# Performance work log

Hardware: AMD Instinct MI355X
Metric: run time of the kernel (lower is better)

## Reference

```python
import jax, jax.numpy as jnp
import numpy as np
import itertools
from jax import lax

B, CIN, COUT, RES, NH = 32, 512, 512, 56, 8
STRIDE = RES // 7  # 8 -> post-stride grid is 7x7 (N=49)
HD = COUT // NH    # 64


def _affine(x, s, b):  # BatchNorm2d in inference form (per-channel scale/shift)
    return x * s[None, :, None, None] + b[None, :, None, None]


def _conv1x1(x, w):  # w: [O, C]
    return jnp.einsum('oc,bchw->bohw', w, x)


def _conv3x3(x, w, stride, groups):
    return lax.conv_general_dilated(
        x, w, window_strides=(stride, stride), padding=[(1, 1), (1, 1)],
        feature_group_count=groups, dimension_numbers=('NCHW', 'OIHW', 'NCHW'))


def _bias_idx():
    points = list(itertools.product(range(7), range(7)))
    offsets, idxs = {}, []
    for p1 in points:
        for p2 in points:
            off = (abs(p1[0] - p2[0]), abs(p1[1] - p2[1]))
            if off not in offsets:
                offsets[off] = len(offsets)
            idxs.append(offsets[off])
    return np.array(idxs, dtype=np.int32).reshape(49, 49), len(offsets)


def setup_inputs() -> dict:
    key = jax.random.key(0)
    ks = jax.random.split(key, 24)
    idx_np, n_off = _bias_idx()  # n_off = 49
    rn = lambda k, sh, sc: jax.random.normal(k, sh, dtype=jnp.float32) * sc
    return {
        'x': rn(ks[0], (B, CIN, RES, RES), 1.0),
        'dw_w': rn(ks[1], (CIN, 1, 3, 3), 0.2),
        'bn0_s': 1.0 + rn(ks[2], (CIN,), 0.05), 'bn0_b': rn(ks[3], (CIN,), 0.05),
        'wq': rn(ks[4], (COUT, CIN), 0.03),
        'bnq_s': 1.0 + rn(ks[5], (COUT,), 0.05), 'bnq_b': rn(ks[6], (COUT,), 0.05),
        'wk': rn(ks[7], (COUT, CIN), 0.03),
        'bnk_s': 1.0 + rn(ks[8], (COUT,), 0.05), 'bnk_b': rn(ks[9], (COUT,), 0.05),
        'wv': rn(ks[10], (COUT, CIN), 0.03),
        'bnv_s': 1.0 + rn(ks[11], (COUT,), 0.05), 'bnv_b': rn(ks[12], (COUT,), 0.05),
        'loc_w': rn(ks[13], (COUT, COUT // NH, 3, 3), 0.05), 'loc_b': rn(ks[14], (COUT,), 0.02),
        'bnl_s': 1.0 + rn(ks[15], (COUT,), 0.05), 'bnl_b': rn(ks[16], (COUT,), 0.05),
        'th1': rn(ks[17], (NH, NH), 0.3), 'th2': rn(ks[18], (NH, NH), 0.3),
        'logit_scale': jnp.log(10.0) * jnp.ones((NH, 1, 1), dtype=jnp.float32),
        'ab': rn(ks[19], (NH, n_off), 0.02),
        'wo': rn(ks[20], (COUT, COUT), 0.03),
        'bno_s': 1.0 + rn(ks[21], (COUT,), 0.05), 'bno_b': rn(ks[22], (COUT,), 0.05),
        'bias_idx': jnp.array(idx_np),
    }


def reference(x, dw_w, bn0_s, bn0_b, wq, bnq_s, bnq_b, wk, bnk_s, bnk_b,
              wv, bnv_s, bnv_b, loc_w, loc_b, bnl_s, bnl_b, th1, th2,
              logit_scale, ab, wo, bno_s, bno_b, bias_idx):
    # stride_conv: depthwise 3x3 stride-8 + BN -> [B, C, 7, 7]
    x = _affine(_conv3x3(x, dw_w, STRIDE, CIN), bn0_s, bn0_b)
    Bc, C, H, W = x.shape
    N = H * W  # 49
    q = _affine(_conv1x1(x, wq), bnq_s, bnq_b).reshape(Bc, NH, HD, N).transpose(0, 1, 3, 2)  # [B,H,N,d]
    k = _affine(_conv1x1(x, wk), bnk_s, bnk_b).reshape(Bc, NH, HD, N)                        # [B,H,d,N]
    v4 = _affine(_conv1x1(x, wv), bnv_s, bnv_b)                                              # [B,Cout,7,7]
    v_local = _affine(_conv3x3(v4, loc_w, 1, NH) + loc_b[None, :, None, None], bnl_s, bnl_b)
    v = v4.reshape(Bc, NH, HD, N).transpose(0, 1, 3, 2)                                      # [B,H,N,d]
    # faithful to source: q normalized over head_dim, k normalized over token axis (last)
    qn = q / jnp.maximum(jnp.linalg.norm(q, axis=-1, keepdims=True), 1e-12)
    kn = k / jnp.maximum(jnp.linalg.norm(k, axis=-1, keepdims=True), 1e-12)
    ls = jnp.exp(jnp.minimum(logit_scale, jnp.log(100.0)))  # clamp max then exp
    attn = jnp.einsum('bhnd,bhdm->bhnm', qn, kn) * ls + ab[:, bias_idx]  # [B,H,49,49]
    attn = jnp.einsum('ij,bjnm->binm', th1, attn)   # talking head 1
    attn = jax.nn.softmax(attn, axis=-1)
    attn = jnp.einsum('ij,bjnm->binm', th2, attn)   # talking head 2
    out = jnp.einsum('bhnm,bhmd->bhnd', attn, v)    # [B,H,N,d]
    out = out.transpose(0, 1, 3, 2).reshape(Bc, COUT, H, W) + v_local
    out = jax.image.resize(out, (Bc, COUT, H * STRIDE, W * STRIDE), method='bilinear')
    out = out * jax.nn.relu6(out + 3.0) / 6.0       # Hardswish
    return _affine(_conv1x1(out, wo), bno_s, bno_b)
```

## Files before the change

kernel.cpp:

```cpp
#include <hip/hip_runtime.h>
#include <hip/hip_bf16.h>
#include <stdint.h>

typedef short short8 __attribute__((ext_vector_type(8)));
typedef float f32x4 __attribute__((ext_vector_type(4)));

#define NB    32
#define NC    512
#define NHD   8
#define HDD   64
#define N7    49
#define RES   56
#define P56   3136
#define NTOK  1568
#define NTOKP 1664
#define NBIG  100352
#define KDIM  512
#define KLOC  576

__device__ __forceinline__ void gload_lds16(const __hip_bfloat16* g, __hip_bfloat16* l) {
  __builtin_amdgcn_global_load_lds(
      (const __attribute__((address_space(1))) void*)g,
      (__attribute__((address_space(3))) void*)l, 16, 0, 0);
}

__global__ __launch_bounds__(256) void k_stride_cvt(
    const float* __restrict__ x, const float* __restrict__ dw,
    const float* __restrict__ s0, const float* __restrict__ b0,
    __hip_bfloat16* __restrict__ xs,
    const float* __restrict__ c0, const float* __restrict__ c1,
    const float* __restrict__ c2, const float* __restrict__ c3,
    const float* __restrict__ c4,
    __hip_bfloat16* __restrict__ d0, __hip_bfloat16* __restrict__ d1,
    __hip_bfloat16* __restrict__ d2, __hip_bfloat16* __restrict__ d3,
    __hip_bfloat16* __restrict__ d4) {
  const int bid = blockIdx.x, t = threadIdx.x;
  if (bid >= 4096) {
    const long base = (long)(bid - 4096) * 2048;
#pragma unroll
    for (int j = 0; j < 8; ++j) {
      long i = base + t + j * 256;
      const float* s; __hip_bfloat16* d; long off;
      if (i >= 1048576)      { s = c4; d = d4; off = i - 1048576; }
      else if (i >= 786432)  { s = c3; d = d3; off = i - 786432; }
      else if (i >= 524288)  { s = c2; d = d2; off = i - 524288; }
      else if (i >= 262144)  { s = c1; d = d1; off = i - 262144; }
      else                   { s = c0; d = d0; off = i; }
      d[off] = __float2bfloat16(s[off]);
    }
    return;
  }
  const int b = bid >> 7, cig = bid & 127;
  const int sub = t >> 6, lane = t & 63;
  const int ci = cig * 4 + sub;
  __shared__ float rows[4][21][56];
  const float* xp = x + ((size_t)(b * NC + ci)) * RES * RES;
  for (int r = lane; r < 21 * 56; r += 64) {
    int rr = r / 56, cc = r - rr * 56;
    int oh = rr / 3, kh = rr - oh * 3;
    int ih = oh * 8 + kh - 1;
    rows[sub][rr][cc] = (ih >= 0) ? xp[ih * 56 + cc] : 0.f;
  }
  float w[9];
#pragma unroll
  for (int j = 0; j < 9; ++j) w[j] = dw[ci * 9 + j];
  const float sc = s0[ci], bi = b0[ci];
  __syncthreads();
  if (lane < 49) {
    const int oh = lane / 7, ow = lane - oh * 7;
    float acc = 0.f;
#pragma unroll
    for (int kh = 0; kh < 3; ++kh)
#pragma unroll
      for (int kw = 0; kw < 3; ++kw) {
        int col = ow * 8 + kw - 1;
        float v = (col >= 0) ? rows[sub][oh * 3 + kh][col] : 0.f;
        acc += v * w[kh * 3 + kw];
      }
    xs[(size_t)(b * 49 + lane) * NC + ci] = __float2bfloat16(acc * sc + bi);
  }
}

__global__ __launch_bounds__(512) void k_gemm_big(
    const __hip_bfloat16* __restrict__ A,
    const __hip_bfloat16* __restrict__ Bm,
    const float* __restrict__ scale, const float* __restrict__ bias,
    float* __restrict__ out) {
  __shared__ __align__(16) __hip_bfloat16 lsA[2][256 * 32];
  __shared__ __align__(16) __hip_bfloat16 lsB[2][256 * 32];
  const int t = threadIdx.x;
  const int cpx = gridDim.x >> 3;
  const int nid = (blockIdx.x & 7) * cpx + (blockIdx.x >> 3);
  const int m0 = (nid & 1) * 256, n0 = (nid >> 1) * 256;

  const int lane = t & 63, wid = t >> 6;
  const int wm = (wid >> 2) * 128, wn = (wid & 3) * 64;
  const int fr = lane & 15, fq = lane >> 4;
  const int rslot = (fq ^ ((fr >> 1) & 3)) * 8;

  const int srow = t >> 2;
  const int scol = ((t & 3) ^ ((t >> 3) & 3)) * 8;
  const __hip_bfloat16* Ab = A  + (size_t)(m0 + srow) * KDIM + scol;
  const __hip_bfloat16* Bb = Bm + (size_t)(n0 + srow) * KDIM + scol;

  const f32x4 fz = {0.f, 0.f, 0.f, 0.f};
  f32x4 acc[8][4];
#pragma unroll
  for (int i = 0; i < 8; ++i)
#pragma unroll
    for (int j = 0; j < 4; ++j) acc[i][j] = fz;

#define STA(tile, call) gload_lds16(Ab + (tile) * 32 + (size_t)(call) * 128 * KDIM, \
                                    lsA[(tile) & 1] + (call) * 4096 + wid * 512)
#define STB(tile, call) gload_lds16(Bb + (tile) * 32 + (size_t)(call) * 128 * KDIM, \
                                    lsB[(tile) & 1] + (call) * 4096 + wid * 512)

  STA(0, 0); STA(0, 1); STB(0, 0); STB(0, 1);
  STA(1, 0); STA(1, 1); STB(1, 0); STB(1, 1);

#pragma unroll 1
  for (int tt = 0; tt < 16; ++tt) {
    if (tt < 15) asm volatile("s_waitcnt vmcnt(4)" ::: "memory");
    else         asm volatile("s_waitcnt vmcnt(0)" ::: "memory");
    __builtin_amdgcn_sched_barrier(0);
    __builtin_amdgcn_s_barrier();
    __builtin_amdgcn_sched_barrier(0);

    const __hip_bfloat16* lA = lsA[tt & 1];
    const __hip_bfloat16* lB = lsB[tt & 1];
    short8 af[4], ag[4], bf[4];
#pragma unroll
    for (int i = 0; i < 4; ++i)
      af[i] = *(const short8*)(lA + (wm + i * 16 + fr) * 32 + rslot);
#pragma unroll
    for (int i = 0; i < 4; ++i)
      ag[i] = *(const short8*)(lA + (wm + 64 + i * 16 + fr) * 32 + rslot);
#pragma unroll
    for (int j = 0; j < 4; ++j)
      bf[j] = *(const short8*)(lB + (wn + j * 16 + fr) * 32 + rslot);
    __builtin_amdgcn_s_setprio(1);
#pragma unroll
    for (int i = 0; i < 4; ++i)
#pragma unroll
      for (int j = 0; j < 4; ++j)
        acc[i][j] = __builtin_amdgcn_mfma_f32_16x16x32_bf16(af[i], bf[j], acc[i][j], 0, 0, 0);
#pragma unroll
    for (int i = 0; i < 4; ++i)
#pragma unroll
      for (int j = 0; j < 4; ++j)
        acc[4 + i][j] = __builtin_amdgcn_mfma_f32_16x16x32_bf16(ag[i], bf[j], acc[4 + i][j], 0, 0, 0);
    __builtin_amdgcn_s_setprio(0);

    __builtin_amdgcn_sched_barrier(0);
    __builtin_amdgcn_s_barrier();
    __builtin_amdgcn_sched_barrier(0);
    if (tt < 14) { STA(tt + 2, 0); STA(tt + 2, 1); STB(tt + 2, 0); STB(tt + 2, 1); }
  }
#undef STA
#undef STB

#pragma unroll
  for (int mi = 0; mi < 8; ++mi) {
#pragma unroll
    for (int ni = 0; ni < 4; ++ni) {
      const int gn = n0 + wn + ni * 16 + fr;
      const int outer = gn / P56;
      const int ii = gn - outer * P56;
#pragma unroll
      for (int r = 0; r < 4; ++r) {
        const int co = m0 + wm + mi * 16 + fq * 4 + r;
        out[((size_t)outer * NC + co) * P56 + ii] = acc[mi][ni][r] * scale[co] + bias[co];
      }
    }
  }
}

__global__ __launch_bounds__(256) void k_gemm_qkv(
    const __hip_bfloat16* __restrict__ wqb, const __hip_bfloat16* __restrict__ wkb,
    const __hip_bfloat16* __restrict__ wvb, const __hip_bfloat16* __restrict__ xs,
    const float* __restrict__ sq, const float* __restrict__ bq,
    const float* __restrict__ sk, const float* __restrict__ bk,
    const float* __restrict__ sv, const float* __restrict__ bv,
    float* __restrict__ qb, float* __restrict__ kb, float* __restrict__ vb) {
  __shared__ __align__(16) __hip_bfloat16 lsA[2][128 * 32];
  __shared__ __align__(16) __hip_bfloat16 lsB[2][128 * 32];
  const int t = threadIdx.x;
  const int nwg = gridDim.x;
  const int orig = blockIdx.x;
  const int q = nwg >> 3, r = nwg & 7;
  const int xcd = orig & 7, pos = orig >> 3;
  const int nid = (xcd < r ? xcd * (q + 1) : r * (q + 1) + (xcd - r) * q) + pos;
  const int mt = nid % 12, nt = nid / 12;
  const int n0 = nt * 128, m0 = (mt & 3) * 128, sel = mt >> 2;

  const __hip_bfloat16* A = (sel == 0 ? wqb : sel == 1 ? wkb : wvb);
  const float* scale = (sel == 0 ? sq : sel == 1 ? sk : sv);
  const float* bias  = (sel == 0 ? bq : sel == 1 ? bk : bv);
  float* out = (sel == 0 ? qb : sel == 1 ? kb : vb);

  const int lane = t & 63, wid = t >> 6;
  const int wm = (wid >> 1) * 64, wn = (wid & 1) * 64;
  const int fr = lane & 15, fq = lane >> 4;
  const int rslot = (fq ^ ((fr >> 1) & 3)) * 8;
  const int srow = t >> 2;
  const int scol = ((t & 3) ^ ((t >> 3) & 3)) * 8;
  const __hip_bfloat16* Ab = A  + (size_t)(m0 + srow) * KDIM + scol;
  const __hip_bfloat16* Bb = xs + (size_t)(n0 + srow) * KDIM + scol;

  const f32x4 fz = {0.f, 0.f, 0.f, 0.f};
  f32x4 acc[4][4];
#pragma unroll
  for (int i = 0; i < 4; ++i)
#pragma unroll
    for (int j = 0; j < 4; ++j) acc[i][j] = fz;

#define STG_QKV(tile)                                                   \
  do {                                                                  \
    const int kof = (tile) * 32; const int bb = (tile) & 1;             \
    gload_lds16(Ab + kof,                       lsA[bb] + wid * 512);   \
    gload_lds16(Ab + kof + (size_t)64 * KDIM,   lsA[bb] + 2048 + wid * 512); \
    gload_lds16(Bb + kof,                       lsB[bb] + wid * 512);   \
    gload_lds16(Bb + kof + (size_t)64 * KDIM,   lsB[bb] + 2048 + wid * 512); \
  } while (0)

  STG_QKV(0);
  STG_QKV(1);
#pragma unroll 1
  for (int it = 0; it < 16; ++it) {
    if (it < 15) asm volatile("s_waitcnt vmcnt(4)" ::: "memory");
    else         asm volatile("s_waitcnt vmcnt(0)" ::: "memory");
    __builtin_amdgcn_sched_barrier(0);
    __builtin_amdgcn_s_barrier();
    __builtin_amdgcn_sched_barrier(0);
    const __hip_bfloat16* lA = lsA[it & 1];
    const __hip_bfloat16* lB = lsB[it & 1];
    short8 af[4], bf[4];
#pragma unroll
    for (int mi = 0; mi < 4; ++mi)
      af[mi] = *(const short8*)(lA + (wm + mi * 16 + fr) * 32 + rslot);
#pragma unroll
    for (int ni = 0; ni < 4; ++ni)
      bf[ni] = *(const short8*)(lB + (wn + ni * 16 + fr) * 32 + rslot);
#pragma unroll
    for (int mi = 0; mi < 4; ++mi)
#pragma unroll
      for (int ni = 0; ni < 4; ++ni)
        acc[mi][ni] = __builtin_amdgcn_mfma_f32_16x16x32_bf16(af[mi], bf[ni], acc[mi][ni], 0, 0, 0);
    __builtin_amdgcn_sched_barrier(0);
    __builtin_amdgcn_s_barrier();
    __builtin_amdgcn_sched_barrier(0);
    if (it < 14) STG_QKV(it + 2);
  }
#undef STG_QKV

#pragma unroll
  for (int mi = 0; mi < 4; ++mi) {
#pragma unroll
    for (int ni = 0; ni < 4; ++ni) {
      const int gn = n0 + wn + ni * 16 + fr;
      if (gn >= NTOK) continue;
      const int b = gn / 49, ii = gn - b * 49;
#pragma unroll
      for (int r = 0; r < 4; ++r) {
        const int co = m0 + wm + mi * 16 + fq * 4 + r;
        out[((size_t)b * NC + co) * 49 + ii] = acc[mi][ni][r] * scale[co] + bias[co];
      }
    }
  }
}

__global__ __launch_bounds__(256) void k_im2col(
    const float* __restrict__ vb, __hip_bfloat16* __restrict__ bloc) {
  const int g = blockIdx.x, b = blockIdx.y, t = threadIdx.x;
  __shared__ __hip_bfloat16 pad[64][81];
  for (int i = t; i < 64 * 81; i += 256) pad[i / 81][i % 81] = __float2bfloat16(0.f);
  __syncthreads();
  const float* src = vb + ((size_t)b * NC + g * 64) * 49;
  for (int i = t; i < 64 * 49; i += 256) {
    const int ci = i / 49, n = i - ci * 49;
    const int oh = n / 7, ow = n - oh * 7;
    pad[ci][(oh + 1) * 9 + (ow + 1)] = __float2bfloat16(src[i]);
  }
  __syncthreads();
  __hip_bfloat16* dst = bloc + ((size_t)g * NTOKP + (size_t)b * 49) * KLOC;
  for (int i8 = t; i8 < 49 * KLOC / 8; i8 += 256) {
    const int i = i8 * 8;
    const int n = i / KLOC, k0 = i - n * KLOC;
    const int oh = n / 7, ow = n - oh * 7;
    short8 pk;
#pragma unroll
    for (int j = 0; j < 8; ++j) {
      const int k = k0 + j;
      const int ci = k / 9, tap = k - ci * 9;
      const int kh = tap / 3, kw = tap - kh * 3;
      pk[j] = (short)__bfloat16_as_ushort(pad[ci][(oh + kh) * 9 + (ow + kw)]);
    }
    *(short8*)(dst + (size_t)n * KLOC + k0) = pk;
  }
}

__global__ __launch_bounds__(256) void k_vloc_gemm(
    const __hip_bfloat16* __restrict__ lwb,
    const __hip_bfloat16* __restrict__ bloc,
    const float* __restrict__ lbias, const float* __restrict__ sl,
    const float* __restrict__ bl, float* __restrict__ vloc) {
  __shared__ __align__(16) __hip_bfloat16 lsA[2][64 * 32];
  __shared__ __align__(16) __hip_bfloat16 lsB[2][128 * 32];
  const int t = threadIdx.x;
  const int g = blockIdx.y;
  const int n0 = blockIdx.x * 128;
  const int lane = t & 63, wid = t >> 6;
  const int wm = (wid >> 1) * 32, wn = (wid & 1) * 64;
  const int fr = lane & 15, fq = lane >> 4;
  const int rslot = (fq ^ ((fr >> 1) & 3)) * 8;
  const int srow = t >> 2;
  const int scol = ((t & 3) ^ ((t >> 3) & 3)) * 8;
  const __hip_bfloat16* Ab = lwb  + ((size_t)g * 64 + srow) * KLOC + scol;
  const __hip_bfloat16* Bb = bloc + ((size_t)g * NTOKP + n0 + srow) * KLOC + scol;

  const f32x4 fz = {0.f, 0.f, 0.f, 0.f};
  f32x4 acc[2][4];
#pragma unroll
  for (int i = 0; i < 2; ++i)
#pragma unroll
    for (int j = 0; j < 4; ++j) acc[i][j] = fz;

#define STG_VL(tile)                                                     \
  do {                                                                   \
    const int kof = (tile) * 32; const int bb = (tile) & 1;              \
    gload_lds16(Ab + kof,                      lsA[bb] + wid * 512);     \
    gload_lds16(Bb + kof,                      lsB[bb] + wid * 512);     \
    gload_lds16(Bb + kof + (size_t)64 * KLOC,  lsB[bb] + 2048 + wid * 512); \
  } while (0)

  STG_VL(0);
  STG_VL(1);
#pragma unroll 1
  for (int it = 0; it < 18; ++it) {
    if (it < 17) asm volatile("s_waitcnt vmcnt(3)" ::: "memory");
    else         asm volatile("s_waitcnt vmcnt(0)" ::: "memory");
    __builtin_amdgcn_sched_barrier(0);
    __builtin_amdgcn_s_barrier();
    __builtin_amdgcn_sched_barrier(0);
    const __hip_bfloat16* lA = lsA[it & 1];
    const __hip_bfloat16* lB = lsB[it & 1];
    short8 af[2], bf[4];
#pragma unroll
    for (int mi = 0; mi < 2; ++mi)
      af[mi] = *(const short8*)(lA + (wm + mi * 16 + fr) * 32 + rslot);
#pragma unroll
    for (int ni = 0; ni < 4; ++ni)
      bf[ni] = *(const short8*)(lB + (wn + ni * 16 + fr) * 32 + rslot);
#pragma unroll
    for (int mi = 0; mi < 2; ++mi)
#pragma unroll
      for (int ni = 0; ni < 4; ++ni)
        acc[mi][ni] = __builtin_amdgcn_mfma_f32_16x16x32_bf16(af[mi], bf[ni], acc[mi][ni], 0, 0, 0);
    __builtin_amdgcn_sched_barrier(0);
    __builtin_amdgcn_s_barrier();
    __builtin_amdgcn_sched_barrier(0);
    if (it < 16) STG_VL(it + 2);
  }
#undef STG_VL

#pragma unroll
  for (int mi = 0; mi < 2; ++mi) {
#pragma unroll
    for (int ni = 0; ni < 4; ++ni) {
      const int gn = n0 + wn + ni * 16 + fr;
      if (gn >= NTOK) continue;
      const int b = gn / 49, n = gn - b * 49;
#pragma unroll
      for (int r = 0; r < 4; ++r) {
        const int oc = g * 64 + wm + mi * 16 + fq * 4 + r;
        const float sc = sl[oc];
        vloc[((size_t)b * NC + oc) * 49 + n] = acc[mi][ni][r] * sc + lbias[oc] * sc + bl[oc];
      }
    }
  }
}

__global__ __launch_bounds__(256) void k_attn1(
    const float* __restrict__ qb, const float* __restrict__ kb,
    const float* __restrict__ lsc, const float* __restrict__ ab, const int* __restrict__ bidx,
    float* __restrict__ Sbuf) {
  const int h = blockIdx.x, b = blockIdx.y, t = threadIdx.x;
  __shared__ float qt[64 * 49], kt[64 * 49], nq[49], abl[49];
  const float* qs = qb + ((size_t)b * NC + h * 64) * 49;
  const float* ks = kb + ((size_t)b * NC + h * 64) * 49;
  for (int i = t; i < 64 * 49; i += 256) { qt[i] = qs[i]; kt[i] = ks[i]; }
  if (t < 49) abl[t] = ab[h * 49 + t];
  __syncthreads();
  if (t < 49) {
    float s = 0.f;
    for (int d = 0; d < 64; ++d) { float v = qt[d * 49 + t]; s += v * v; }
    nq[t] = fmaxf(sqrtf(s), 1e-12f);
  } else if (t >= 64 && t < 128) {
    const int d = t - 64;
    float s = 0.f;
    for (int m = 0; m < 49; ++m) { float v = kt[d * 49 + m]; s += v * v; }
    const float inv = 1.f / fmaxf(sqrtf(s), 1e-12f);
    for (int m = 0; m < 49; ++m) kt[d * 49 + m] *= inv;
  }
  __syncthreads();
  const float ls = expf(fminf(lsc[h], logf(100.f)));
  for (int idx = t; idx < 49 * 49; idx += 256) {
    const int n = idx / 49, m = idx - n * 49;
    float acc = 0.f;
    for (int d = 0; d < 64; ++d) acc += qt[d * 49 + n] * kt[d * 49 + m];
    Sbuf[(((size_t)b * NHD + h) * 49 + n) * 49 + m] = acc / nq[n] * ls + abl[bidx[idx]];
  }
}

__global__ __launch_bounds__(256) void k_attn2(
    const float* __restrict__ Sbuf, const float* __restrict__ th1, const float* __restrict__ th2,
    const float* __restrict__ vb, const float* __restrict__ vloc, float* __restrict__ y7) {
  const int n = blockIdx.x, b = blockIdx.y, t = threadIdx.x;
  __shared__ float sS[8][49], sP[8][49], sQ[8][49];
  __shared__ float t1[64], t2[64], rsuminv[8];
  if (t < 64) { t1[t] = th1[t]; t2[t] = th2[t]; }
  for (int i = t; i < 392; i += 256) {
    const int j = i / 49, m = i - j * 49;
    sS[j][m] = Sbuf[(((size_t)b * NHD + j) * 49 + n) * 49 + m];
  }
  __syncthreads();
  for (int i = t; i < 392; i += 256) {
    const int j = i / 49, m = i - j * 49;
    float a = 0.f;
#pragma unroll
    for (int jj = 0; jj < 8; ++jj) a += t1[j * 8 + jj] * sS[jj][m];
    sP[j][m] = a;
  }
  __syncthreads();
  if (t < 8) {
    float mx = -1e30f;
    for (int m = 0; m < 49; ++m) mx = fmaxf(mx, sP[t][m]);
    float s = 0.f;
    for (int m = 0; m < 49; ++m) { float e = expf(sP[t][m] - mx); sP[t][m] = e; s += e; }
    rsuminv[t] = 1.f / s;
  }
  __syncthreads();
  for (int i = t; i < 392; i += 256) {
    const int j = i / 49, m = i - j * 49;
    float a = 0.f;
#pragma unroll
    for (int jj = 0; jj < 8; ++jj) a += t2[j * 8 + jj] * (sP[jj][m] * rsuminv[jj]);
    sQ[j][m] = a;
  }
  __syncthreads();
  for (int c = t; c < NC; c += 256) {
    const int hh = c >> 6;
    const float* vp = vb + ((size_t)b * NC + c) * 49;
    float a = 0.f;
    for (int m = 0; m < 49; ++m) a += sQ[hh][m] * vp[m];
    a += vloc[((size_t)b * NC + c) * 49 + n];
    y7[((size_t)b * 49 + n) * NC + c] = a;
  }
}

__global__ __launch_bounds__(256) void k_resize(const float* __restrict__ y7,
                                                __hip_bfloat16* __restrict__ h) {
  const int y = blockIdx.x, b = blockIdx.y, t = threadIdx.x;
  __shared__ float L[2][7][512];
  float sy = (y - 3.5f) * 0.125f;
  sy = fminf(fmaxf(sy, 0.f), 6.f);
  const int iy0 = min((int)floorf(sy), 5);
  const float wy = sy - (float)iy0;
  const float* src = y7 + ((size_t)b * 49 + iy0 * 7) * NC;
  float* Lf = &L[0][0][0];
  for (int i = t; i < 2 * 7 * 512; i += 256) Lf[i] = src[i];
  __syncthreads();
  const size_t outb = ((size_t)b * P56 + (size_t)y * 56) * NC;
  const int cg = (t & 63) * 8;
  const int xq = t >> 6;
  for (int x0 = 0; x0 < 56; x0 += 4) {
    const int x = x0 + xq;
    float sx = (x - 3.5f) * 0.125f;
    sx = fminf(fmaxf(sx, 0.f), 6.f);
    const int ix0 = min((int)floorf(sx), 5);
    const float wx = sx - (float)ix0;
    const float w00 = (1.f - wy) * (1.f - wx), w01 = (1.f - wy) * wx;
    const float w10 = wy * (1.f - wx),         w11 = wy * wx;
    short8 pk;
#pragma unroll
    for (int j = 0; j < 8; ++j) {
      const int c = cg + j;
      const float v = w00 * L[0][ix0][c] + w01 * L[0][ix0 + 1][c]
                    + w10 * L[1][ix0][c] + w11 * L[1][ix0 + 1][c];
      const float hs = v * fminf(fmaxf(v + 3.f, 0.f), 6.f) * (1.f / 6.f);
      pk[j] = (short)__bfloat16_as_ushort(__float2bfloat16(hs));
    }
    *(short8*)(&h[outb + (size_t)x * NC + cg]) = pk;
  }
}

extern "C" void kernel_launch(void* const* d_in, const int* in_sizes, int n_in,
                              void* d_out, int out_size, void* d_ws, size_t ws_size,
                              hipStream_t stream) {
  (void)in_sizes; (void)n_in; (void)out_size; (void)ws_size;
  const float* x     = (const float*)d_in[0];
  const float* dw_w  = (const float*)d_in[1];
  const float* bn0_s = (const float*)d_in[2];
  const float* bn0_b = (const float*)d_in[3];
  const float* wq    = (const float*)d_in[4];
  const float* bnq_s = (const float*)d_in[5];
  const float* bnq_b = (const float*)d_in[6];
  const float* wk    = (const float*)d_in[7];
  const float* bnk_s = (const float*)d_in[8];
  const float* bnk_b = (const float*)d_in[9];
  const float* wv    = (const float*)d_in[10];
  const float* bnv_s = (const float*)d_in[11];
  const float* bnv_b = (const float*)d_in[12];
  const float* loc_w = (const float*)d_in[13];
  const float* loc_b = (const float*)d_in[14];
  const float* bnl_s = (const float*)d_in[15];
  const float* bnl_b = (const float*)d_in[16];
  const float* th1   = (const float*)d_in[17];
  const float* th2   = (const float*)d_in[18];
  const float* lsc   = (const float*)d_in[19];
  const float* ab    = (const float*)d_in[20];
  const float* wo    = (const float*)d_in[21];
  const float* bno_s = (const float*)d_in[22];
  const float* bno_b = (const float*)d_in[23];
  const int*   bidx  = (const int*)d_in[24];

  char* w = (char*)d_ws;
  auto alloc = [&](size_t bytes) {
    char* p = w;
    w += (bytes + 255) & ~(size_t)255;
    return p;
  };
  __hip_bfloat16* h_buf = (__hip_bfloat16*)alloc((size_t)NBIG * NC * 2);
  __hip_bfloat16* wq_b  = (__hip_bfloat16*)alloc((size_t)NC * NC * 2);
  __hip_bfloat16* wk_b  = (__hip_bfloat16*)alloc((size_t)NC * NC * 2);
  __hip_bfloat16* wv_b  = (__hip_bfloat16*)alloc((size_t)NC * NC * 2);
  __hip_bfloat16* wo_b  = (__hip_bfloat16*)alloc((size_t)NC * NC * 2);
  __hip_bfloat16* lw_b  = (__hip_bfloat16*)alloc((size_t)NC * KLOC * 2);
  __hip_bfloat16* xs    = (__hip_bfloat16*)alloc((size_t)NTOKP * NC * 2);
  float* qb   = (float*)alloc((size_t)NB * NC * 49 * 4);
  float* kb   = (float*)alloc((size_t)NB * NC * 49 * 4);
  float* vb   = (float*)alloc((size_t)NB * NC * 49 * 4);
  float* vloc = (float*)alloc((size_t)NB * NC * 49 * 4);
  float* y7   = (float*)alloc((size_t)NB * 49 * NC * 4);
  float* Sb   = (float*)alloc((size_t)NB * NHD * 49 * 49 * 4);
  __hip_bfloat16* bloc = (__hip_bfloat16*)h_buf;

  k_stride_cvt<<<dim3(4096 + 656), 256, 0, stream>>>(
      x, dw_w, bn0_s, bn0_b, xs,
      wq, wk, wv, wo, loc_w, wq_b, wk_b, wv_b, wo_b, lw_b);
  k_gemm_qkv<<<dim3(13 * 12), 256, 0, stream>>>(wq_b, wk_b, wv_b, xs,
                                                bnq_s, bnq_b, bnk_s, bnk_b, bnv_s, bnv_b,
                                                qb, kb, vb);
  k_im2col<<<dim3(NHD, NB), 256, 0, stream>>>(vb, bloc);
  k_vloc_gemm<<<dim3(13, NHD), 256, 0, stream>>>(lw_b, bloc, loc_b, bnl_s, bnl_b, vloc);
  k_attn1<<<dim3(NHD, NB), 256, 0, stream>>>(qb, kb, lsc, ab, bidx, Sb);
  k_attn2<<<dim3(49, NB), 256, 0, stream>>>(Sb, th1, th2, vb, vloc, y7);
  k_resize<<<dim3(RES, NB), 256, 0, stream>>>(y7, h_buf);
  k_gemm_big<<<dim3(784), 512, 0, stream>>>(wo_b, h_buf, bno_s, bno_b, (float*)d_out);
}
```

Measured before the change: 260.3 us.

## Merge independent mid-stage kernels into two heterogeneous launches, fold vloc add into resize

Combines attn1 with im2col and attn2 with the local-conv GEMM into two launches whose blocks branch on blockIdx, so independent work runs concurrently and two kernel launches and their boundaries disappear. The vloc output is now written token-major and added during the resize load instead of inside attn2, which removes the dependency between them. The heterogeneous blocks take the larger shared-memory footprint of either branch, which can lower occupancy, and the vloc writes are now strided by channel.

```diff
diff --git a/kernel.cpp b/kernel.cpp
--- a/kernel.cpp
+++ b/kernel.cpp
@@ -269,196 +269,207 @@
   }
 }
 
-__global__ __launch_bounds__(256) void k_im2col(
+__global__ __launch_bounds__(256) void k_mid1(
+    const float* __restrict__ qb, const float* __restrict__ kb,
+    const float* __restrict__ lsc, const float* __restrict__ ab, const int* __restrict__ bidx,
+    float* __restrict__ Sbuf,
     const float* __restrict__ vb, __hip_bfloat16* __restrict__ bloc) {
-  const int g = blockIdx.x, b = blockIdx.y, t = threadIdx.x;
-  __shared__ __hip_bfloat16 pad[64][81];
-  for (int i = t; i < 64 * 81; i += 256) pad[i / 81][i % 81] = __float2bfloat16(0.f);
-  __syncthreads();
-  const float* src = vb + ((size_t)b * NC + g * 64) * 49;
-  for (int i = t; i < 64 * 49; i += 256) {
-    const int ci = i / 49, n = i - ci * 49;
-    const int oh = n / 7, ow = n - oh * 7;
-    pad[ci][(oh + 1) * 9 + (ow + 1)] = __float2bfloat16(src[i]);
-  }
-  __syncthreads();
-  __hip_bfloat16* dst = bloc + ((size_t)g * NTOKP + (size_t)b * 49) * KLOC;
-  for (int i8 = t; i8 < 49 * KLOC / 8; i8 += 256) {
-    const int i = i8 * 8;
-    const int n = i / KLOC, k0 = i - n * KLOC;
-    const int oh = n / 7, ow = n - oh * 7;
-    short8 pk;
-#pragma unroll
-    for (int j = 0; j < 8; ++j) {
-      const int k = k0 + j;
-      const int ci = k / 9, tap = k - ci * 9;
-      const int kh = tap / 3, kw = tap - kh * 3;
-      pk[j] = (short)__bfloat16_as_ushort(pad[ci][(oh + kh) * 9 + (ow + kw)]);
-    }
-    *(short8*)(dst + (size_t)n * KLOC + k0) = pk;
-  }
-}
-
-__global__ __launch_bounds__(256) void k_vloc_gemm(
-    const __hip_bfloat16* __restrict__ lwb,
-    const __hip_bfloat16* __restrict__ bloc,
+  __shared__ __align__(16) char smem[25792];
+  const int bid = blockIdx.x, t = threadIdx.x;
+  if (bid < 256) {
+    const int h = bid & 7, b = bid >> 3;
+    float* qt  = (float*)smem;
+    float* kt  = qt + 3136;
+    float* nq  = kt + 3136;
+    float* abl = nq + 49;
+    const float* qs = qb + ((size_t)b * NC + h * 64) * 49;
+    const float* ks = kb + ((size_t)b * NC + h * 64) * 49;
+    for (int i = t; i < 64 * 49; i += 256) { qt[i] = qs[i]; kt[i] = ks[i]; }
+    if (t < 49) abl[t] = ab[h * 49 + t];
+    __syncthreads();
+    if (t < 49) {
+      float s = 0.f;
+      for (int d = 0; d < 64; ++d) { float v = qt[d * 49 + t]; s += v * v; }
+      nq[t] = fmaxf(sqrtf(s), 1e-12f);
+    } else if (t >= 64 && t < 128) {
+      const int d = t - 64;
+      float s = 0.f;
+      for (int m = 0; m < 49; ++m) { float v = kt[d * 49 + m]; s += v * v; }
+      const float inv = 1.f / fmaxf(sqrtf(s), 1e-12f);
+      for (int m = 0; m < 49; ++m) kt[d * 49 + m] *= inv;
+    }
+    __syncthreads();
+    const float ls = expf(fminf(lsc[h], logf(100.f)));
+    for (int idx = t; idx < 49 * 49; idx += 256) {
+      const int n = idx / 49, m = idx - n * 49;
+      float acc = 0.f;
+      for (int d = 0; d < 64; ++d) acc += qt[d * 49 + n] * kt[d * 49 + m];
+      Sbuf[(((size_t)b * NHD + h) * 49 + n) * 49 + m] = acc / nq[n] * ls + abl[bidx[idx]];
+    }
+  } else {
+    const int i2 = bid - 256;
+    const int g = i2 & 7, b = i2 >> 3;
+    __hip_bfloat16* pad = (__hip_bfloat16*)smem;
+    for (int i = t; i < 64 * 81; i += 256) pad[i] = __float2bfloat16(0.f);
+    __syncthreads();
+    const float* src = vb + ((size_t)b * NC + g * 64) * 49;
+    for (int i = t; i < 64 * 49; i += 256) {
+      const int ci = i / 49, n = i - ci * 49;
+      const int oh = n / 7, ow = n - oh * 7;
+      pad[ci * 81 + (oh + 1) * 9 + (ow + 1)] = __float2bfloat16(src[i]);
+    }
+    __syncthreads();
+    __hip_bfloat16* dst = bloc + ((size_t)g * NTOKP + (size_t)b * 49) * KLOC;
+    for (int i8 = t; i8 < 49 * KLOC / 8; i8 += 256) {
+      const int i = i8 * 8;
+      const int n = i / KLOC, k0 = i - n * KLOC;
+      const int oh = n / 7, ow = n - oh * 7;
+      short8 pk;
+#pragma unroll
+      for (int j = 0; j < 8; ++j) {
+        const int k = k0 + j;
+        const int ci = k / 9, tap = k - ci * 9;
+        const int kh = tap / 3, kw = tap - kh * 3;
+        pk[j] = (short)__bfloat16_as_ushort(pad[ci * 81 + (oh + kh) * 9 + (ow + kw)]);
+      }
+      *(short8*)(dst + (size_t)n * KLOC + k0) = pk;
+    }
+  }
+}
+
+__global__ __launch_bounds__(256) void k_mid2(
+    const float* __restrict__ Sbuf, const float* __restrict__ th1, const float* __restrict__ th2,
+    const float* __restrict__ vb, float* __restrict__ y7,
+    const __hip_bfloat16* __restrict__ lwb, const __hip_bfloat16* __restrict__ bloc,
     const float* __restrict__ lbias, const float* __restrict__ sl,
     const float* __restrict__ bl, float* __restrict__ vloc) {
-  __shared__ __align__(16) __hip_bfloat16 lsA[2][64 * 32];
-  __shared__ __align__(16) __hip_bfloat16 lsB[2][128 * 32];
-  const int t = threadIdx.x;
-  const int g = blockIdx.y;
-  const int n0 = blockIdx.x * 128;
-  const int lane = t & 63, wid = t >> 6;
-  const int wm = (wid >> 1) * 32, wn = (wid & 1) * 64;
-  const int fr = lane & 15, fq = lane >> 4;
-  const int rslot = (fq ^ ((fr >> 1) & 3)) * 8;
-  const int srow = t >> 2;
-  const int scol = ((t & 3) ^ ((t >> 3) & 3)) * 8;
-  const __hip_bfloat16* Ab = lwb  + ((size_t)g * 64 + srow) * KLOC + scol;
-  const __hip_bfloat16* Bb = bloc + ((size_t)g * NTOKP + n0 + srow) * KLOC + scol;
-
-  const f32x4 fz = {0.f, 0.f, 0.f, 0.f};
-  f32x4 acc[2][4];
-#pragma unroll
-  for (int i = 0; i < 2; ++i)
-#pragma unroll
-    for (int j = 0; j < 4; ++j) acc[i][j] = fz;
-
-#define STG_VL(tile)                                                     \
-  do {                                                                   \
-    const int kof = (tile) * 32; const int bb = (tile) & 1;              \
-    gload_lds16(Ab + kof,                      lsA[bb] + wid * 512);     \
-    gload_lds16(Bb + kof,                      lsB[bb] + wid * 512);     \
-    gload_lds16(Bb + kof + (size_t)64 * KLOC,  lsB[bb] + 2048 + wid * 512); \
+  __shared__ __align__(16) char smem[24576];
+  const int bid = blockIdx.x, t = threadIdx.x;
+  if (bid < 1568) {
+    const int n = bid % 49, b = bid / 49;
+    float* sS = (float*)smem;
+    float* sP = sS + 392;
+    float* sQ = sP + 392;
+    float* t1 = sQ + 392;
+    float* t2 = t1 + 64;
+    float* rsuminv = t2 + 64;
+    if (t < 64) { t1[t] = th1[t]; t2[t] = th2[t]; }
+    for (int i = t; i < 392; i += 256) {
+      const int j = i / 49, m = i - j * 49;
+      sS[j * 49 + m] = Sbuf[(((size_t)b * NHD + j) * 49 + n) * 49 + m];
+    }
+    __syncthreads();
+    for (int i = t; i < 392; i += 256) {
+      const int j = i / 49, m = i - j * 49;
+      float a = 0.f;
+#pragma unroll
+      for (int jj = 0; jj < 8; ++jj) a += t1[j * 8 + jj] * sS[jj * 49 + m];
+      sP[j * 49 + m] = a;
+    }
+    __syncthreads();
+    if (t < 8) {
+      float mx = -1e30f;
+      for (int m = 0; m < 49; ++m) mx = fmaxf(mx, sP[t * 49 + m]);
+      float s = 0.f;
+      for (int m = 0; m < 49; ++m) { float e = expf(sP[t * 49 + m] - mx); sP[t * 49 + m] = e; s += e; }
+      rsuminv[t] = 1.f / s;
+    }
+    __syncthreads();
+    for (int i = t; i < 392; i += 256) {
+      const int j = i / 49, m = i - j * 49;
+      float a = 0.f;
+#pragma unroll
+      for (int jj = 0; jj < 8; ++jj) a += t2[j * 8 + jj] * (sP[jj * 49 + m] * rsuminv[jj]);
+      sQ[j * 49 + m] = a;
+    }
+    __syncthreads();
+    for (int c = t; c < NC; c += 256) {
+      const int hh = c >> 6;
+      const float* vp = vb + ((size_t)b * NC + c) * 49;
+      float a = 0.f;
+      for (int m = 0; m < 49; ++m) a += sQ[hh * 49 + m] * vp[m];
+      y7[((size_t)b * 49 + n) * NC + c] = a;
+    }
+  } else {
+    const int i2 = bid - 1568;
+    const int n0 = (i2 % 13) * 128;
+    const int g = i2 / 13;
+    __hip_bfloat16* lsA = (__hip_bfloat16*)smem;
+    __hip_bfloat16* lsB = lsA + 4096;
+    const int lane = t & 63, wid = t >> 6;
+    const int wm = (wid >> 1) * 32, wn = (wid & 1) * 64;
+    const int fr = lane & 15, fq = lane >> 4;
+    const int rslot = (fq ^ ((fr >> 1) & 3)) * 8;
+    const int srow = t >> 2;
+    const int scol = ((t & 3) ^ ((t >> 3) & 3)) * 8;
+    const __hip_bfloat16* Ab = lwb  + ((size_t)g * 64 + srow) * KLOC + scol;
+    const __hip_bfloat16* Bb = bloc + ((size_t)g * NTOKP + n0 + srow) * KLOC + scol;
+
+    const f32x4 fz = {0.f, 0.f, 0.f, 0.f};
+    f32x4 acc[2][4];
+#pragma unroll
+    for (int i = 0; i < 2; ++i)
+#pragma unroll
+      for (int j = 0; j < 4; ++j) acc[i][j] = fz;
+
+#define STG_VL(tile)                                                      \
+  do {                                                                    \
+    const int kof = (tile) * 32; const int bb = (tile) & 1;               \
+    gload_lds16(Ab + kof,                      lsA + bb * 2048 + wid * 512); \
+    gload_lds16(Bb + kof,                      lsB + bb * 4096 + wid * 512); \
+    gload_lds16(Bb + kof + (size_t)64 * KLOC,  lsB + bb * 4096 + 2048 + wid * 512); \
   } while (0)
 
-  STG_VL(0);
-  STG_VL(1);
+    STG_VL(0);
+    STG_VL(1);
 #pragma unroll 1
-  for (int it = 0; it < 18; ++it) {
-    if (it < 17) asm volatile("s_waitcnt vmcnt(3)" ::: "memory");
-    else         asm volatile("s_waitcnt vmcnt(0)" ::: "memory");
-    __builtin_amdgcn_sched_barrier(0);
-    __builtin_amdgcn_s_barrier();
-    __builtin_amdgcn_sched_barrier(0);
-    const __hip_bfloat16* lA = lsA[it & 1];
-    const __hip_bfloat16* lB = lsB[it & 1];
-    short8 af[2], bf[4];
-#pragma unroll
-    for (int mi = 0; mi < 2; ++mi)
-      af[mi] = *(const short8*)(lA + (wm + mi * 16 + fr) * 32 + rslot);
-#pragma unroll
-    for (int ni = 0; ni < 4; ++ni)
-      bf[ni] = *(const short8*)(lB + (wn + ni * 16 + fr) * 32 + rslot);
-#pragma unroll
-    for (int mi = 0; mi < 2; ++mi)
+    for (int it = 0; it < 18; ++it) {
+      if (it < 17) asm volatile("s_waitcnt vmcnt(3)" ::: "memory");
+      else         asm volatile("s_waitcnt vmcnt(0)" ::: "memory");
+      __builtin_amdgcn_sched_barrier(0);
+      __builtin_amdgcn_s_barrier();
+      __builtin_amdgcn_sched_barrier(0);
+      const __hip_bfloat16* lA = lsA + (it & 1) * 2048;
+      const __hip_bfloat16* lB = lsB + (it & 1) * 4096;
+      short8 af[2], bf[4];
+#pragma unroll
+      for (int mi = 0; mi < 2; ++mi)
+        af[mi] = *(const short8*)(lA + (wm + mi * 16 + fr) * 32 + rslot);
 #pragma unroll
       for (int ni = 0; ni < 4; ++ni)
-        acc[mi][ni] = __builtin_amdgcn_mfma_f32_16x16x32_bf16(af[mi], bf[ni], acc[mi][ni], 0, 0, 0);
-    __builtin_amdgcn_sched_barrier(0);
-    __builtin_amdgcn_s_barrier();
-    __builtin_amdgcn_sched_barrier(0);
-    if (it < 16) STG_VL(it + 2);
-  }
+        bf[ni] = *(const short8*)(lB + (wn + ni * 16 + fr) * 32 + rslot);
+#pragma unroll
+      for (int mi = 0; mi < 2; ++mi)
+#pragma unroll
+        for (int ni = 0; ni < 4; ++ni)
+          acc[mi][ni] = __builtin_amdgcn_mfma_f32_16x16x32_bf16(af[mi], bf[ni], acc[mi][ni], 0, 0, 0);
+      __builtin_amdgcn_sched_barrier(0);
+      __builtin_amdgcn_s_barrier();
+      __builtin_amdgcn_sched_barrier(0);
+      if (it < 16) STG_VL(it + 2);
+    }
 #undef STG_VL
 
 #pragma unroll
-  for (int mi = 0; mi < 2; ++mi) {
-#pragma unroll
-    for (int ni = 0; ni < 4; ++ni) {
-      const int gn = n0 + wn + ni * 16 + fr;
-      if (gn >= NTOK) continue;
-      const int b = gn / 49, n = gn - b * 49;
-#pragma unroll
-      for (int r = 0; r < 4; ++r) {
-        const int oc = g * 64 + wm + mi * 16 + fq * 4 + r;
-        const float sc = sl[oc];
-        vloc[((size_t)b * NC + oc) * 49 + n] = acc[mi][ni][r] * sc + lbias[oc] * sc + bl[oc];
+    for (int mi = 0; mi < 2; ++mi) {
+#pragma unroll
+      for (int ni = 0; ni < 4; ++ni) {
+        const int gn = n0 + wn + ni * 16 + fr;
+        if (gn >= NTOK) continue;
+        const int b = gn / 49, n = gn - b * 49;
+#pragma unroll
+        for (int r = 0; r < 4; ++r) {
+          const int oc = g * 64 + wm + mi * 16 + fq * 4 + r;
+          const float sc = sl[oc];
+          vloc[((size_t)b * 49 + n) * NC + oc] = acc[mi][ni][r] * sc + lbias[oc] * sc + bl[oc];
+        }
       }
     }
   }
 }
 
-__global__ __launch_bounds__(256) void k_attn1(
-    const float* __restrict__ qb, const float* __restrict__ kb,
-    const float* __restrict__ lsc, const float* __restrict__ ab, const int* __restrict__ bidx,
-    float* __restrict__ Sbuf) {
-  const int h = blockIdx.x, b = blockIdx.y, t = threadIdx.x;
-  __shared__ float qt[64 * 49], kt[64 * 49], nq[49], abl[49];
-  const float* qs = qb + ((size_t)b * NC + h * 64) * 49;
-  const float* ks = kb + ((size_t)b * NC + h * 64) * 49;
-  for (int i = t; i < 64 * 49; i += 256) { qt[i] = qs[i]; kt[i] = ks[i]; }
-  if (t < 49) abl[t] = ab[h * 49 + t];
-  __syncthreads();
-  if (t < 49) {
-    float s = 0.f;
-    for (int d = 0; d < 64; ++d) { float v = qt[d * 49 + t]; s += v * v; }
-    nq[t] = fmaxf(sqrtf(s), 1e-12f);
-  } else if (t >= 64 && t < 128) {
-    const int d = t - 64;
-    float s = 0.f;
-    for (int m = 0; m < 49; ++m) { float v = kt[d * 49 + m]; s += v * v; }
-    const float inv = 1.f / fmaxf(sqrtf(s), 1e-12f);
-    for (int m = 0; m < 49; ++m) kt[d * 49 + m] *= inv;
-  }
-  __syncthreads();
-  const float ls = expf(fminf(lsc[h], logf(100.f)));
-  for (int idx = t; idx < 49 * 49; idx += 256) {
-    const int n = idx / 49, m = idx - n * 49;
-    float acc = 0.f;
-    for (int d = 0; d < 64; ++d) acc += qt[d * 49 + n] * kt[d * 49 + m];
-    Sbuf[(((size_t)b * NHD + h) * 49 + n) * 49 + m] = acc / nq[n] * ls + abl[bidx[idx]];
-  }
-}
-
-__global__ __launch_bounds__(256) void k_attn2(
-    const float* __restrict__ Sbuf, const float* __restrict__ th1, const float* __restrict__ th2,
-    const float* __restrict__ vb, const float* __restrict__ vloc, float* __restrict__ y7) {
-  const int n = blockIdx.x, b = blockIdx.y, t = threadIdx.x;
-  __shared__ float sS[8][49], sP[8][49], sQ[8][49];
-  __shared__ float t1[64], t2[64], rsuminv[8];
-  if (t < 64) { t1[t] = th1[t]; t2[t] = th2[t]; }
-  for (int i = t; i < 392; i += 256) {
-    const int j = i / 49, m = i - j * 49;
-    sS[j][m] = Sbuf[(((size_t)b * NHD + j) * 49 + n) * 49 + m];
-  }
-  __syncthreads();
-  for (int i = t; i < 392; i += 256) {
-    const int j = i / 49, m = i - j * 49;
-    float a = 0.f;
-#pragma unroll
-    for (int jj = 0; jj < 8; ++jj) a += t1[j * 8 + jj] * sS[jj][m];
-    sP[j][m] = a;
-  }
-  __syncthreads();
-  if (t < 8) {
-    float mx = -1e30f;
-    for (int m = 0; m < 49; ++m) mx = fmaxf(mx, sP[t][m]);
-    float s = 0.f;
-    for (int m = 0; m < 49; ++m) { float e = expf(sP[t][m] - mx); sP[t][m] = e; s += e; }
-    rsuminv[t] = 1.f / s;
-  }
-  __syncthreads();
-  for (int i = t; i < 392; i += 256) {
-    const int j = i / 49, m = i - j * 49;
-    float a = 0.f;
-#pragma unroll
-    for (int jj = 0; jj < 8; ++jj) a += t2[j * 8 + jj] * (sP[jj][m] * rsuminv[jj]);
-    sQ[j][m] = a;
-  }
-  __syncthreads();
-  for (int c = t; c < NC; c += 256) {
-    const int hh = c >> 6;
-    const float* vp = vb + ((size_t)b * NC + c) * 49;
-    float a = 0.f;
-    for (int m = 0; m < 49; ++m) a += sQ[hh][m] * vp[m];
-    a += vloc[((size_t)b * NC + c) * 49 + n];
-    y7[((size_t)b * 49 + n) * NC + c] = a;
-  }
-}
-
 __global__ __launch_bounds__(256) void k_resize(const float* __restrict__ y7,
+                                                const float* __restrict__ vloc,
                                                 __hip_bfloat16* __restrict__ h) {
   const int y = blockIdx.x, b = blockIdx.y, t = threadIdx.x;
   __shared__ float L[2][7][512];
@@ -466,9 +477,11 @@
   sy = fminf(fmaxf(sy, 0.f), 6.f);
   const int iy0 = min((int)floorf(sy), 5);
   const float wy = sy - (float)iy0;
-  const float* src = y7 + ((size_t)b * 49 + iy0 * 7) * NC;
+  const size_t rowoff = ((size_t)b * 49 + iy0 * 7) * NC;
+  const float* src  = y7 + rowoff;
+  const float* vsrc = vloc + rowoff;
   float* Lf = &L[0][0][0];
-  for (int i = t; i < 2 * 7 * 512; i += 256) Lf[i] = src[i];
+  for (int i = t; i < 2 * 7 * 512; i += 256) Lf[i] = src[i] + vsrc[i];
   __syncthreads();
   const size_t outb = ((size_t)b * P56 + (size_t)y * 56) * NC;
   const int cg = (t & 63) * 8;
@@ -540,7 +553,7 @@
   float* qb   = (float*)alloc((size_t)NB * NC * 49 * 4);
   float* kb   = (float*)alloc((size_t)NB * NC * 49 * 4);
   float* vb   = (float*)alloc((size_t)NB * NC * 49 * 4);
-  float* vloc = (float*)alloc((size_t)NB * NC * 49 * 4);
+  float* vloc = (float*)alloc((size_t)NB * 49 * NC * 4);
   float* y7   = (float*)alloc((size_t)NB * 49 * NC * 4);
   float* Sb   = (float*)alloc((size_t)NB * NHD * 49 * 49 * 4);
   __hip_bfloat16* bloc = (__hip_bfloat16*)h_buf;
@@ -551,10 +564,9 @@
   k_gemm_qkv<<<dim3(13 * 12), 256, 0, stream>>>(wq_b, wk_b, wv_b, xs,
                                                 bnq_s, bnq_b, bnk_s, bnk_b, bnv_s, bnv_b,
                                                 qb, kb, vb);
-  k_im2col<<<dim3(NHD, NB), 256, 0, stream>>>(vb, bloc);
-  k_vloc_gemm<<<dim3(13, NHD), 256, 0, stream>>>(lw_b, bloc, loc_b, bnl_s, bnl_b, vloc);
-  k_attn1<<<dim3(NHD, NB), 256, 0, stream>>>(qb, kb, lsc, ab, bidx, Sb);
-  k_attn2<<<dim3(49, NB), 256, 0, stream>>>(Sb, th1, th2, vb, vloc, y7);
-  k_resize<<<dim3(RES, NB), 256, 0, stream>>>(y7, h_buf);
+  k_mid1<<<dim3(512), 256, 0, stream>>>(qb, kb, lsc, ab, bidx, Sb, vb, bloc);
+  k_mid2<<<dim3(1568 + 104), 256, 0, stream>>>(Sb, th1, th2, vb, y7,
+                                               lw_b, bloc, loc_b, bnl_s, bnl_b, vloc);
+  k_resize<<<dim3(RES, NB), 256, 0, stream>>>(y7, vloc, h_buf);
   k_gemm_big<<<dim3(784), 512, 0, stream>>>(wo_b, h_buf, bno_s, bno_b, (float*)d_out);
 }
```

Measured after the change: 240.5 us. 1.08x faster.
